# Performance work log

Measured on AMD Instinct MI355X. Metric: run time of the kernel, lower is better.

Reference implementation:

```python
import jax, jax.numpy as jnp
import numpy as np

B, S, D, H, FF = 4, 1024, 1024, 16, 4096
DH = D // H
EPS = 1e-5


def setup_inputs() -> dict:
    key = jax.random.key(0)
    ks = jax.random.split(key, 24)
    w = lambda i, shp: jax.random.normal(ks[i], shp, jnp.float32) * 0.02
    inp = {
        'tgt': jax.random.normal(ks[0], (B, S, D), jnp.float32),
        'memory': jax.random.normal(ks[1], (B, S, D), jnp.float32),
        'mask': jax.random.randint(ks[2], (B, S, S), 0, 2, jnp.int32),
        # self-attention projections (stored [in,out]; torch Linear weight transposed)
        'sa_wq': w(3, (D, D)), 'sa_bq': jnp.zeros((D,), jnp.float32),
        'sa_wk': w(4, (D, D)), 'sa_bk': jnp.zeros((D,), jnp.float32),
        'sa_wv': w(5, (D, D)), 'sa_bv': jnp.zeros((D,), jnp.float32),
        'sa_wo': w(6, (D, D)), 'sa_bo': jnp.zeros((D,), jnp.float32),
        # cross-attention projections
        'ca_wq': w(7, (D, D)), 'ca_bq': jnp.zeros((D,), jnp.float32),
        'ca_wk': w(8, (D, D)), 'ca_bk': jnp.zeros((D,), jnp.float32),
        'ca_wv': w(9, (D, D)), 'ca_bv': jnp.zeros((D,), jnp.float32),
        'ca_wo': w(10, (D, D)), 'ca_bo': jnp.zeros((D,), jnp.float32),
        # FFN
        'w1': w(11, (D, FF)), 'b1': jnp.zeros((FF,), jnp.float32),
        'w2': w(12, (FF, D)), 'b2': jnp.zeros((D,), jnp.float32),
        # LayerNorms
        'g1': jnp.ones((D,), jnp.float32), 'be1': jnp.zeros((D,), jnp.float32),
        'g2': jnp.ones((D,), jnp.float32), 'be2': jnp.zeros((D,), jnp.float32),
        'g3': jnp.ones((D,), jnp.float32), 'be3': jnp.zeros((D,), jnp.float32),
    }
    return inp


def _layernorm(x, g, b):
    m = jnp.mean(x, axis=-1, keepdims=True)
    v = jnp.mean((x - m) ** 2, axis=-1, keepdims=True)
    return (x - m) * jax.lax.rsqrt(v + EPS) * g + b


def _mha(x, y, mask, wq, bq, wk, bk, wv, bv, wo, bo):
    # chunk(h,-1)+cat(0) head-split == reshape to [B,S,H,DH]
    b_, sq, _ = x.shape
    sk = y.shape[1]
    q = (x @ wq + bq).reshape(b_, sq, H, DH)
    k = (y @ wk + bk).reshape(b_, sk, H, DH)
    v = (y @ wv + bv).reshape(b_, sk, H, DH)
    score = jnp.einsum('bqhd,bkhd->bhqk', q, k) / jnp.float32(np.sqrt(DH))
    score = score + (1.0 - mask[:, None].astype(score.dtype)) * (-1e9)
    attn = jax.nn.softmax(score, axis=-1)
    out = jnp.einsum('bhqk,bkhd->bqhd', attn, v).reshape(b_, sq, D)
    return out @ wo + bo


def reference(tgt, memory, mask,
              sa_wq, sa_bq, sa_wk, sa_bk, sa_wv, sa_bv, sa_wo, sa_bo,
              ca_wq, ca_bq, ca_wk, ca_bk, ca_wv, ca_bv, ca_wo, ca_bo,
              w1, b1, w2, b2, g1, be1, g2, be2, g3, be3):
    t = tgt + _mha(tgt, tgt, mask, sa_wq, sa_bq, sa_wk, sa_bk, sa_wv, sa_bv, sa_wo, sa_bo)
    t = _layernorm(t, g1, be1)
    t = t + _mha(t, memory, mask, ca_wq, ca_bq, ca_wk, ca_bk, ca_wv, ca_bv, ca_wo, ca_bo)
    t = _layernorm(t, g2, be2)
    t = t + (jax.nn.relu(t @ w1 + b1) @ w2 + b2)
    t = _layernorm(t, g3, be3)
    return t
```

## Files before the change

kernel.cpp:

```cpp
#include <hip/hip_runtime.h>
#include <math.h>

typedef float f32x4 __attribute__((ext_vector_type(4)));
typedef unsigned short ushort8 __attribute__((ext_vector_type(8)));
typedef unsigned short ushort4v __attribute__((ext_vector_type(4)));
typedef __bf16 bf16x8 __attribute__((ext_vector_type(8)));
typedef unsigned int u32;

__device__ __forceinline__ unsigned short f2bf(float x) {
  union { float f; unsigned u; } v; v.f = x;
  unsigned r = v.u + 0x7FFFu + ((v.u >> 16) & 1u);
  return (unsigned short)(r >> 16);
}
__device__ __forceinline__ float bf2f(unsigned short u) {
  union { unsigned u; float f; } c; c.u = ((unsigned)u) << 16; return c.f;
}

__device__ __forceinline__ f32x4 mfma16(ushort8 a, ushort8 b, f32x4 c) {
  return __builtin_amdgcn_mfma_f32_16x16x32_bf16(
      __builtin_bit_cast(bf16x8, a), __builtin_bit_cast(bf16x8, b), c, 0, 0, 0);
}

__device__ __forceinline__ void gload16(const void* g, void* l) {
  __builtin_amdgcn_global_load_lds((const __attribute__((address_space(1))) u32*)g,
                                   (__attribute__((address_space(3))) u32*)l, 16, 0, 0);
}

__global__ __launch_bounds__(256) void gemm_bf16_kernel(
    const unsigned short* __restrict__ A, const unsigned short* __restrict__ Bt,
    const float* __restrict__ bias, void* __restrict__ C,
    int M, int N, int K, int flags)
{
  __shared__ __align__(16) char As0[128 * 128];
  __shared__ __align__(16) char Bs0[128 * 128];
  __shared__ __align__(16) char As1[128 * 128];
  __shared__ __align__(16) char Bs1[128 * 128];
  const int bn = blockIdx.x, bm = blockIdx.y;
  const int t = threadIdx.x;
  const int lane = t & 63, w = t >> 6, wm = w >> 1, wn = w & 1;
  const int l4 = lane & 15, lg = lane >> 4;
  const size_t K2 = (size_t)K * 2;

  f32x4 acc[4][4];
#pragma unroll
  for (int i = 0; i < 4; ++i)
#pragma unroll
    for (int j = 0; j < 4; ++j) acc[i][j] = f32x4{0.f, 0.f, 0.f, 0.f};

  const int lr = lane >> 3;
  const int ls = (lane & 7) ^ lr;
  const char* Ag = (const char*)A + (size_t)(bm * 128 + w * 32 + lr) * K2 + ls * 16;
  const char* Bg = (const char*)Bt + (size_t)(bn * 128 + w * 32 + lr) * K2 + ls * 16;
  const int wo = w * 4096;

  auto STAGE = [&](char* Al, char* Bl, int kt) {
    const size_t ko = (size_t)kt * 128;
#pragma unroll
    for (int i = 0; i < 4; ++i) {
      gload16(Ag + i * 8 * K2 + ko, Al + wo + i * 1024);
      gload16(Bg + i * 8 * K2 + ko, Bl + wo + i * 1024);
    }
  };
  auto COMPUTE = [&](const char* As, const char* Bs) {
#pragma unroll
    for (int ks = 0; ks < 2; ++ks) {
      const int kb = ks * 64 + lg * 16;
      ushort8 af[4], bfr[4];
#pragma unroll
      for (int mi = 0; mi < 4; ++mi) {
        int r = wm * 64 + mi * 16 + l4;
        af[mi] = *reinterpret_cast<const ushort8*>(As + r * 128 + (kb ^ ((r & 7) << 4)));
      }
#pragma unroll
      for (int ni = 0; ni < 4; ++ni) {
        int r = wn * 64 + ni * 16 + l4;
        bfr[ni] = *reinterpret_cast<const ushort8*>(Bs + r * 128 + (kb ^ ((r & 7) << 4)));
      }
#pragma unroll
      for (int mi = 0; mi < 4; ++mi)
#pragma unroll
        for (int ni = 0; ni < 4; ++ni)
          acc[mi][ni] = mfma16(af[mi], bfr[ni], acc[mi][ni]);
    }
  };

  const int nkt = K >> 6;
  STAGE(As0, Bs0, 0);
  __syncthreads();
  for (int kt = 0; kt < nkt; kt += 2) {
    STAGE(As1, Bs1, kt + 1);
    COMPUTE(As0, Bs0);
    __syncthreads();
    if (kt + 2 < nkt) STAGE(As0, Bs0, kt + 2);
    COMPUTE(As1, Bs1);
    __syncthreads();
  }

  const int relu = flags & 1, obf = flags & 2;
#pragma unroll
  for (int mi = 0; mi < 4; ++mi)
#pragma unroll
    for (int ni = 0; ni < 4; ++ni) {
      int col = bn * 128 + wn * 64 + ni * 16 + l4;
      float bia = bias[col];
#pragma unroll
      for (int j = 0; j < 4; ++j) {
        int row = bm * 128 + wm * 64 + mi * 16 + lg * 4 + j;
        float vv = acc[mi][ni][j] + bia;
        if (relu) vv = fmaxf(vv, 0.f);
        if (obf) ((unsigned short*)C)[(size_t)row * N + col] = f2bf(vv);
        else     ((float*)C)[(size_t)row * N + col] = vv;
      }
    }
}

constexpr int kS = 1024, kD = 1024, kDH = 64;

__global__ __launch_bounds__(256) void attn_kernel(
    const unsigned short* __restrict__ Qg, const unsigned short* __restrict__ Kg,
    const unsigned short* __restrict__ Vg, int qs, int ks_,
    const unsigned short* __restrict__ mpack, unsigned short* __restrict__ Og)
{
  __shared__ __align__(16) char Ks0[8192];
  __shared__ __align__(16) char Ks1[8192];
  __shared__ __align__(16) char VT0[8192];
  __shared__ __align__(16) char VT1[8192];
  __shared__ __align__(16) char Ps[8192];
  const int qt = blockIdx.x, h = blockIdx.y, b = blockIdx.z;
  const int t = threadIdx.x, lane = t & 63, w = t >> 6;
  const int l4 = lane & 15, lg = lane >> 4;
  const int lr = lane >> 3, sg = (lane & 7) ^ lr;

  ushort8 q0, q1;
  {
    const unsigned short* src = Qg + (size_t)(b * kS + qt * 64 + w * 16 + l4) * qs + h * kDH;
    q0 = *reinterpret_cast<const ushort8*>(src + lg * 8);
    q1 = *reinterpret_cast<const ushort8*>(src + 32 + lg * 8);
  }
  const unsigned short* mtb = mpack + (size_t)(b * 16 + qt) * 4096 + t;

  auto stageK = [&](char* Kl, int kt) {
    const char* base = (const char*)(Kg + (size_t)(b * kS + kt * 64) * ks_ + h * kDH) + sg * 16;
    gload16(base + (size_t)(w * 16 + lr) * (ks_ * 2), Kl + w * 2048);
    gload16(base + (size_t)(w * 16 + 8 + lr) * (ks_ * 2), Kl + w * 2048 + 1024);
  };

  float m_r[4], l_p[4];
  f32x4 o[4];
#pragma unroll
  for (int j = 0; j < 4; ++j) { m_r[j] = -1e30f; l_p[j] = 0.f; }
#pragma unroll
  for (int di = 0; di < 4; ++di) o[di] = f32x4{0.f, 0.f, 0.f, 0.f};

  ushort8 vA0, vA1, vB0, vB1;
  unsigned short mA, mB;
  stageK(Ks0, 0);
  {
    const unsigned short* vsrc = Vg + (size_t)(b * kS + (t >> 2)) * ks_ + h * kDH + (t & 3) * 16;
    vA0 = *reinterpret_cast<const ushort8*>(vsrc);
    vA1 = *reinterpret_cast<const ushort8*>(vsrc + 8);
    mA = mtb[0];
  }

#define ATTN_TILE(KC, VC, KN, VC0, VC1, VN0, VN1, MCUR, MNXT, KTV)                       \
  {                                                                                      \
    asm volatile("s_waitcnt vmcnt(0)" ::: "memory");                                     \
    {       \
      int key2 = (t >> 2) * 2, c0 = (t & 3) * 16;                                        \
      _Pragma("unroll")                                                                  \
      for (int i = 0; i < 8; ++i) {                                                      \
        int dh = c0 + i;                                                                 \
        *(unsigned short*)(VC + dh * 128 +                                               \
            (key2 ^ ((dh & 7) << 4) ^ ((dh >> 4) << 5))) = VC0[i];                       \
      }                                                                                  \
      _Pragma("unroll")                                                                  \
      for (int i = 0; i < 8; ++i) {                                                      \
        int dh = c0 + 8 + i;                                                             \
        *(unsigned short*)(VC + dh * 128 +                                               \
            (key2 ^ ((dh & 7) << 4) ^ ((dh >> 4) << 5))) = VC1[i];                       \
      }                                                                                  \
    }                                                                                    \
    asm volatile("s_waitcnt lgkmcnt(0)" ::: "memory");                                   \
    __builtin_amdgcn_s_barrier();                                                        \
    __builtin_amdgcn_sched_barrier(0);                                                   \
    if ((KTV) + 1 < 16) {                  \
      stageK(KN, (KTV) + 1);                                                             \
      const unsigned short* vsrc = Vg +                                                  \
          (size_t)(b * kS + ((KTV) + 1) * 64 + (t >> 2)) * ks_ + h * kDH + (t & 3) * 16; \
      VN0 = *reinterpret_cast<const ushort8*>(vsrc);                                     \
      VN1 = *reinterpret_cast<const ushort8*>(vsrc + 8);                                 \
      MNXT = mtb[((KTV) + 1) * 256];                                                     \
    }                                                                                    \
    f32x4 sc[4];                                                                         \
    _Pragma("unroll")                                                                    \
    for (int ni = 0; ni < 4; ++ni) sc[ni] = f32x4{0.f, 0.f, 0.f, 0.f};                   \
    __builtin_amdgcn_s_setprio(1);                                                       \
    _Pragma("unroll")                                                                    \
    for (int ks = 0; ks < 2; ++ks) {                                                     \
      const int kb = ks * 64 + lg * 16;                                                  \
      ushort8 a = ks ? q1 : q0;                                                          \
      _Pragma("unroll")                                                                  \
      for (int ni = 0; ni < 4; ++ni) {                                                   \
        int kr = ni * 16 + l4;                                                           \
        ushort8 bb = *(const ushort8*)(KC + kr * 128 + (kb ^ ((kr & 7) << 4)));          \
        sc[ni] = mfma16(a, bb, sc[ni]);                                                  \
      }                                                                                  \
    }                                                                                    \
    __builtin_amdgcn_s_setprio(0);                                                       \
    const unsigned mbits_ = (unsigned)(MCUR);                                            \
    float tmax[4];                                                                       \
    _Pragma("unroll")                                                                    \
    for (int j = 0; j < 4; ++j) {                                                        \
      _Pragma("unroll")                                                                  \
      for (int ni = 0; ni < 4; ++ni)                                                     \
        if (!((mbits_ >> (ni * 4 + j)) & 1u)) sc[ni][j] = -1e9f;                         \
      tmax[j] = fmaxf(fmaxf(sc[0][j], sc[1][j]), fmaxf(sc[2][j], sc[3][j]));             \
    }                                                                                    \
    bool need = (tmax[0] > m_r[0] + 8.f) || (tmax[1] > m_r[1] + 8.f) ||                  \
                (tmax[2] > m_r[2] + 8.f) || (tmax[3] > m_r[3] + 8.f);                    \
    if (__any(need)) {                 \
      _Pragma("unroll")                                                                  \
      for (int j = 0; j < 4; ++j) {                                                      \
        tmax[j] = fmaxf(tmax[j], __shfl_xor(tmax[j], 1, 64));                            \
        tmax[j] = fmaxf(tmax[j], __shfl_xor(tmax[j], 2, 64));                            \
        tmax[j] = fmaxf(tmax[j], __shfl_xor(tmax[j], 4, 64));                            \
        tmax[j] = fmaxf(tmax[j], __shfl_xor(tmax[j], 8, 64));                            \
        float mn = fmaxf(m_r[j], tmax[j]);                                               \
        float al = exp2f(m_r[j] - mn);                                                   \
        m_r[j] = mn; l_p[j] *= al;                                                       \
        o[0][j] *= al; o[1][j] *= al; o[2][j] *= al; o[3][j] *= al;                      \
      }                                                                                  \
    }                                                                                    \
    _Pragma("unroll")                                                                    \
    for (int ni = 0; ni < 4; ++ni)                                                       \
      _Pragma("unroll")                                                                  \
      for (int j = 0; j < 4; ++j) {                                                      \
        float p = exp2f(sc[ni][j] - m_r[j]);                                             \
        sc[ni][j] = p;                                                                   \
        l_p[j] += p;                                                                     \
      }                                                                                  \
    {                               \
      char* Pw = Ps + w * 2048;                                                          \
      _Pragma("unroll")                                                                  \
      for (int ni = 0; ni < 4; ++ni)                                                     \
        _Pragma("unroll")                                                                \
        for (int j = 0; j < 4; ++j) {                                                    \
          int row = lg * 4 + j, col = ni * 16 + l4;                                      \
          *(unsigned short*)(Pw + row * 128 +                                            \
              ((col * 2) ^ ((row & 7) << 4) ^ ((row & 8) << 2))) =                       \
              __builtin_bit_cast(unsigned short, (__bf16)sc[ni][j]);                     \
        }                                                                                \
    }                                                                                    \
    asm volatile("s_waitcnt lgkmcnt(0)" ::: "memory");                                   \
    __builtin_amdgcn_sched_barrier(0);                                                   \
    __builtin_amdgcn_s_setprio(1);                                                       \
    {                      \
      const char* Pw = Ps + w * 2048;                                                    \
      _Pragma("unroll")                                                                  \
      for (int ks = 0; ks < 2; ++ks) {                                                   \
        const int kb = ks * 64 + lg * 16;                                                \
        ushort8 pa = *(const ushort8*)(Pw + l4 * 128 +                                   \
            (kb ^ ((l4 & 7) << 4) ^ ((l4 & 8) << 2)));                                   \
        _Pragma("unroll")                                                                \
        for (int di = 0; di < 4; ++di) {                                                 \
          int vr2 = di * 16 + l4;                                                        \
          ushort8 vb = *(const ushort8*)(VC + vr2 * 128 +                                \
              (kb ^ ((vr2 & 7) << 4) ^ ((vr2 >> 4) << 5)));                              \
          o[di] = mfma16(pa, vb, o[di]);                                                 \
        }                                                                                \
      }                                                                                  \
    }                                                                                    \
    __builtin_amdgcn_s_setprio(0);                                                       \
  }

  for (int kt = 0; kt < 16; kt += 2) {
    ATTN_TILE(Ks0, VT0, Ks1, vA0, vA1, vB0, vB1, mA, mB, kt);
    ATTN_TILE(Ks1, VT1, Ks0, vB0, vB1, vA0, vA1, mB, mA, kt + 1);
  }
#undef ATTN_TILE

  float rinv[4];
#pragma unroll
  for (int j = 0; j < 4; ++j) {
    float s = l_p[j];
    s += __shfl_xor(s, 1, 64);
    s += __shfl_xor(s, 2, 64);
    s += __shfl_xor(s, 4, 64);
    s += __shfl_xor(s, 8, 64);
    rinv[j] = 1.0f / s;
  }
#pragma unroll
  for (int di = 0; di < 4; ++di) {
    int col = h * kDH + di * 16 + l4;
#pragma unroll
    for (int j = 0; j < 4; ++j) {
      int qrow = qt * 64 + w * 16 + lg * 4 + j;
      Og[(size_t)(b * kS + qrow) * kD + col] =
          __builtin_bit_cast(unsigned short, (__bf16)(o[di][j] * rinv[j]));
    }
  }
}

__global__ __launch_bounds__(256) void addln_kernel(
    const float* __restrict__ x, const unsigned short* __restrict__ y,
    const float* __restrict__ g, const float* __restrict__ be,
    float* __restrict__ out, unsigned short* __restrict__ ob)
{
  const int row = blockIdx.x, t = threadIdx.x;
  const size_t base = (size_t)row * 1024 + t * 4;
  float4 xv = *reinterpret_cast<const float4*>(x + base);
  ushort4v yv = *reinterpret_cast<const ushort4v*>(y + base);
  float v0 = xv.x + bf2f(yv[0]), v1 = xv.y + bf2f(yv[1]);
  float v2 = xv.z + bf2f(yv[2]), v3 = xv.w + bf2f(yv[3]);
  float s1 = v0 + v1 + v2 + v3;
  float s2 = v0 * v0 + v1 * v1 + v2 * v2 + v3 * v3;
#pragma unroll
  for (int off = 1; off < 64; off <<= 1) {
    s1 += __shfl_xor(s1, off, 64);
    s2 += __shfl_xor(s2, off, 64);
  }
  __shared__ float r1[4], r2[4];
  const int w = t >> 6, lane = t & 63;
  if (lane == 0) { r1[w] = s1; r2[w] = s2; }
  __syncthreads();
  s1 = r1[0] + r1[1] + r1[2] + r1[3];
  s2 = r2[0] + r2[1] + r2[2] + r2[3];
  const float mean = s1 * (1.0f / 1024.0f);
  const float var = s2 * (1.0f / 1024.0f) - mean * mean;
  const float rs = rsqrtf(var + 1e-5f);
  float4 gv = *reinterpret_cast<const float4*>(g + t * 4);
  float4 bv = *reinterpret_cast<const float4*>(be + t * 4);
  float4 ov;
  ov.x = (v0 - mean) * rs * gv.x + bv.x;
  ov.y = (v1 - mean) * rs * gv.y + bv.y;
  ov.z = (v2 - mean) * rs * gv.z + bv.z;
  ov.w = (v3 - mean) * rs * gv.w + bv.w;
  *reinterpret_cast<float4*>(out + base) = ov;
  if (ob) {
    ushort4v bo;
    bo[0] = f2bf(ov.x); bo[1] = f2bf(ov.y); bo[2] = f2bf(ov.z); bo[3] = f2bf(ov.w);
    *reinterpret_cast<ushort4v*>(ob + base) = bo;
  }
}

__global__ __launch_bounds__(256) void cvt2_bf16_kernel(
    const float* __restrict__ a, const float* __restrict__ b,
    unsigned short* __restrict__ da, unsigned short* __restrict__ db, int n8each)
{
  int i = blockIdx.x * 256 + threadIdx.x;
  const float* s = a; unsigned short* d = da;
  if (i >= n8each) { s = b; d = db; i -= n8each; }
  if (i >= n8each) return;
  float4 f0 = reinterpret_cast<const float4*>(s)[i * 2];
  float4 f1 = reinterpret_cast<const float4*>(s)[i * 2 + 1];
  ushort8 v;
  v[0] = f2bf(f0.x); v[1] = f2bf(f0.y); v[2] = f2bf(f0.z); v[3] = f2bf(f0.w);
  v[4] = f2bf(f1.x); v[5] = f2bf(f1.y); v[6] = f2bf(f1.z); v[7] = f2bf(f1.w);
  reinterpret_cast<ushort8*>(d)[i] = v;
}

__global__ __launch_bounds__(256) void transpose_cvt_kernel(
    const float* __restrict__ src, unsigned short* __restrict__ dst, int K, int N)
{
  __shared__ float tile[32][33];
  const int bx = blockIdx.x, by = blockIdx.y;
  const int tx = threadIdx.x & 31, ty = threadIdx.x >> 5;
#pragma unroll
  for (int i = 0; i < 4; ++i)
    tile[ty + i * 8][tx] = src[(size_t)(by * 32 + ty + i * 8) * N + bx * 32 + tx];
  __syncthreads();
#pragma unroll
  for (int i = 0; i < 4; ++i)
    dst[(size_t)(bx * 32 + ty + i * 8) * K + by * 32 + tx] = f2bf(tile[tx][ty + i * 8]);
}

struct TPtrs { const float* s[8]; unsigned short* d[8]; float scale[8]; };
__global__ __launch_bounds__(256) void tcvt_batch_kernel(TPtrs p)
{
  __shared__ float tile[32][33];
  const float* __restrict__ src = p.s[blockIdx.z];
  unsigned short* __restrict__ dst = p.d[blockIdx.z];
  const float sc = p.scale[blockIdx.z];
  const int bx = blockIdx.x, by = blockIdx.y;
  const int tx = threadIdx.x & 31, ty = threadIdx.x >> 5;
#pragma unroll
  for (int i = 0; i < 4; ++i)
    tile[ty + i * 8][tx] = src[(size_t)(by * 32 + ty + i * 8) * 1024 + bx * 32 + tx];
  __syncthreads();
#pragma unroll
  for (int i = 0; i < 4; ++i)
    dst[(size_t)(bx * 32 + ty + i * 8) * 1024 + by * 32 + tx] = f2bf(tile[tx][ty + i * 8] * sc);
}

__global__ void biasprep_kernel(const float* sq, const float* sk, const float* sv,
                                const float* cq, const float* ck, const float* cv,
                                float* bsa, float* bca, float* bcq, float s)
{
  int i = blockIdx.x * 256 + threadIdx.x;
  if (i < 1024) { bsa[i] = sq[i] * s; bcq[i] = cq[i] * s; bca[i] = ck[i]; bca[i + 1024] = cv[i]; }
  else if (i < 2048) bsa[i] = sk[i - 1024];
  else if (i < 3072) bsa[i] = sv[i - 2048];
}

__global__ __launch_bounds__(256) void maskprep_kernel(
    const int* __restrict__ mask, unsigned short* __restrict__ mpack)
{
  int idx = blockIdx.x * 256 + threadIdx.x;
  int t = idx & 255;
  int kt = (idx >> 8) & 15;
  int qt = (idx >> 12) & 15;
  int b = idx >> 16;
  int qb = qt * 64 + ((t >> 6) & 3) * 16 + ((t >> 4) & 3) * 4;
  int kb = kt * 64 + (t & 15);
  unsigned m = 0;
#pragma unroll
  for (int ni = 0; ni < 4; ++ni)
#pragma unroll
    for (int j = 0; j < 4; ++j)
      if (mask[(size_t)(b * 1024 + qb + j) * 1024 + kb + ni * 16]) m |= 1u << (ni * 4 + j);
  mpack[idx] = (unsigned short)m;
}

extern "C" void kernel_launch(void* const* d_in, const int* in_sizes, int n_in,
                              void* d_out, int out_size, void* d_ws, size_t ws_size,
                              hipStream_t stream)
{
  const float* tgt  = (const float*)d_in[0];
  const float* memi = (const float*)d_in[1];
  const int*   mask = (const int*)d_in[2];
  const float* sa_wq = (const float*)d_in[3];  const float* sa_bq = (const float*)d_in[4];
  const float* sa_wk = (const float*)d_in[5];  const float* sa_bk = (const float*)d_in[6];
  const float* sa_wv = (const float*)d_in[7];  const float* sa_bv = (const float*)d_in[8];
  const float* sa_wo = (const float*)d_in[9];  const float* sa_bo = (const float*)d_in[10];
  const float* ca_wq = (const float*)d_in[11]; const float* ca_bq = (const float*)d_in[12];
  const float* ca_wk = (const float*)d_in[13]; const float* ca_bk = (const float*)d_in[14];
  const float* ca_wv = (const float*)d_in[15]; const float* ca_bv = (const float*)d_in[16];
  const float* ca_wo = (const float*)d_in[17]; const float* ca_bo = (const float*)d_in[18];
  const float* w1 = (const float*)d_in[19]; const float* b1 = (const float*)d_in[20];
  const float* w2 = (const float*)d_in[21]; const float* b2 = (const float*)d_in[22];
  const float* g1 = (const float*)d_in[23]; const float* be1 = (const float*)d_in[24];
  const float* g2 = (const float*)d_in[25]; const float* be2 = (const float*)d_in[26];
  const float* g3 = (const float*)d_in[27]; const float* be3 = (const float*)d_in[28];
  float* out = (float*)d_out;
  char* W = (char*)d_ws;
  const size_t MB = 1 << 20;
  typedef unsigned short us;
  const float QSCALE = 0.18033688011112042f;

  us* Wsaqkv = (us*)(W + 0);
  us* Wsao   = (us*)(W + 6 * MB);
  us* Wcaq   = (us*)(W + 8 * MB);
  us* Wcakv  = (us*)(W + 10 * MB);
  us* Wcao   = (us*)(W + 14 * MB);
  us* W1t    = (us*)(W + 16 * MB);
  us* W2t    = (us*)(W + 24 * MB);
  float* b_saqkv = (float*)(W + 32 * MB);
  float* b_cakv  = (float*)(W + 32 * MB + 16384);
  float* b_caq   = (float*)(W + 32 * MB + 32768);
  us* tgt_bf = (us*)(W + 33 * MB);
  us* T2b    = tgt_bf;
  us* mem_bf = (us*)(W + 41 * MB);
  us* QKV    = (us*)(W + 49 * MB);
  us* Qca    = (us*)(W + 49 * MB);
  us* KVca   = (us*)(W + 57 * MB);
  us* T1b    = (us*)(W + 65 * MB);
  us* AO     = (us*)(W + 73 * MB);
  us* Hb     = (us*)(W + 49 * MB);
  us* Opb    = (us*)(W + 81 * MB);
  us* mpack  = (us*)(W + 89 * MB);
  float* T1f = (float*)(W + 98 * MB);
  float* T2f = T1f;

  const int M = 4096;
  dim3 blk(256);
  auto gemm = [&](const us* Aa, const us* Bta, const float* bias, void* Cc,
                  int Nn, int Kk, int flags) {
    gemm_bf16_kernel<<<dim3(Nn / 128, M / 128), blk, 0, stream>>>(Aa, Bta, bias, Cc, M, Nn, Kk, flags);
  };

  TPtrs tp;
  tp.s[0] = sa_wq; tp.d[0] = Wsaqkv;              tp.scale[0] = QSCALE;
  tp.s[1] = sa_wk; tp.d[1] = Wsaqkv + 1024 * 1024; tp.scale[1] = 1.f;
  tp.s[2] = sa_wv; tp.d[2] = Wsaqkv + 2048 * 1024; tp.scale[2] = 1.f;
  tp.s[3] = sa_wo; tp.d[3] = Wsao;                 tp.scale[3] = 1.f;
  tp.s[4] = ca_wq; tp.d[4] = Wcaq;                 tp.scale[4] = QSCALE;
  tp.s[5] = ca_wk; tp.d[5] = Wcakv;                tp.scale[5] = 1.f;
  tp.s[6] = ca_wv; tp.d[6] = Wcakv + 1024 * 1024;  tp.scale[6] = 1.f;
  tp.s[7] = ca_wo; tp.d[7] = Wcao;                 tp.scale[7] = 1.f;
  tcvt_batch_kernel<<<dim3(32, 32, 8), blk, 0, stream>>>(tp);
  transpose_cvt_kernel<<<dim3(128, 32), blk, 0, stream>>>(w1, W1t, 1024, 4096);
  transpose_cvt_kernel<<<dim3(32, 128), blk, 0, stream>>>(w2, W2t, 4096, 1024);
  cvt2_bf16_kernel<<<dim3(4096), blk, 0, stream>>>(tgt, memi, tgt_bf, mem_bf, M * 1024 / 8);
  biasprep_kernel<<<dim3(12), blk, 0, stream>>>(sa_bq, sa_bk, sa_bv, ca_bq, ca_bk, ca_bv,
                                                b_saqkv, b_cakv, b_caq, QSCALE);
  maskprep_kernel<<<dim3(1024), blk, 0, stream>>>(mask, mpack);

  gemm(tgt_bf, Wsaqkv, b_saqkv, QKV, 3072, 1024, 2);
  attn_kernel<<<dim3(16, 16, 4), blk, 0, stream>>>(QKV, QKV + 1024, QKV + 2048, 3072, 3072, mpack, AO);
  gemm(AO, Wsao, sa_bo, Opb, 1024, 1024, 2);
  addln_kernel<<<dim3(M), blk, 0, stream>>>(tgt, Opb, g1, be1, T1f, T1b);

  gemm(T1b, Wcaq, b_caq, Qca, 1024, 1024, 2);
  gemm(mem_bf, Wcakv, b_cakv, KVca, 2048, 1024, 2);
  attn_kernel<<<dim3(16, 16, 4), blk, 0, stream>>>(Qca, KVca, KVca + 1024, 1024, 2048, mpack, AO);
  gemm(AO, Wcao, ca_bo, Opb, 1024, 1024, 2);
  addln_kernel<<<dim3(M), blk, 0, stream>>>(T1f, Opb, g2, be2, T2f, T2b);

  gemm(T2b, W1t, b1, Hb, 4096, 1024, 3);
  gemm(Hb, W2t, b2, Opb, 1024, 4096, 2);
  addln_kernel<<<dim3(M), blk, 0, stream>>>(T2f, Opb, g3, be3, out, nullptr);

  (void)in_sizes; (void)n_in; (void)out_size; (void)ws_size;
}
```

Baseline: 411.6 us.

## Remap workgroups per XCD and deepen GEMM load pipeline with explicit vmcnt waits

Adds an XCD-aware block index remapping to both the GEMM and attention kernels, so consecutive tiles that share operands land on the same XCD and reuse its L2. The GEMM main loop now issues two stages of global-to-LDS loads ahead and waits with partial s_waitcnt vmcnt instead of full __syncthreads, keeping one tile of loads in flight during compute. This relies on the vmcnt count of 8 matching the number of loads per stage, and the hand-placed barriers carry a risk of LDS races if that assumption does not hold.

```diff
diff --git a/kernel.cpp b/kernel.cpp
--- a/kernel.cpp
+++ b/kernel.cpp
@@ -26,6 +26,12 @@
                                    (__attribute__((address_space(3))) u32*)l, 16, 0, 0);
 }
 
+__device__ __forceinline__ int xcd_swz(int orig, int nwg) {
+  int q = nwg >> 3, r = nwg & 7;
+  int xcd = orig & 7, lid = orig >> 3;
+  return (xcd < r ? xcd * (q + 1) : r * (q + 1) + (xcd - r) * q) + lid;
+}
+
 __global__ __launch_bounds__(256) void gemm_bf16_kernel(
     const unsigned short* __restrict__ A, const unsigned short* __restrict__ Bt,
     const float* __restrict__ bias, void* __restrict__ C,
@@ -35,7 +41,9 @@
   __shared__ __align__(16) char Bs0[128 * 128];
   __shared__ __align__(16) char As1[128 * 128];
   __shared__ __align__(16) char Bs1[128 * 128];
-  const int bn = blockIdx.x, bm = blockIdx.y;
+  const int gx = gridDim.x;
+  const int wg = xcd_swz(blockIdx.x + gx * blockIdx.y, gx * gridDim.y);
+  const int bn = wg % gx, bm = wg / gx;
   const int t = threadIdx.x;
   const int lane = t & 63, w = t >> 6, wm = w >> 1, wn = w & 1;
   const int l4 = lane & 15, lg = lane >> 4;
@@ -84,17 +92,29 @@
     }
   };
 
+#define GWAIT(more) do { if (more) asm volatile("s_waitcnt vmcnt(8)" ::: "memory"); \
+                         else      asm volatile("s_waitcnt vmcnt(0)" ::: "memory"); } while (0)
+
   const int nkt = K >> 6;
   STAGE(As0, Bs0, 0);
-  __syncthreads();
+  STAGE(As1, Bs1, 1);
   for (int kt = 0; kt < nkt; kt += 2) {
-    STAGE(As1, Bs1, kt + 1);
+    GWAIT(kt + 1 < nkt);
+    __builtin_amdgcn_s_barrier();
+    __builtin_amdgcn_sched_barrier(0);
     COMPUTE(As0, Bs0);
-    __syncthreads();
+    __builtin_amdgcn_s_barrier();
+    __builtin_amdgcn_sched_barrier(0);
     if (kt + 2 < nkt) STAGE(As0, Bs0, kt + 2);
+    GWAIT(kt + 2 < nkt);
+    __builtin_amdgcn_s_barrier();
+    __builtin_amdgcn_sched_barrier(0);
     COMPUTE(As1, Bs1);
-    __syncthreads();
-  }
+    __builtin_amdgcn_s_barrier();
+    __builtin_amdgcn_sched_barrier(0);
+    if (kt + 3 < nkt) STAGE(As1, Bs1, kt + 3);
+  }
+#undef GWAIT
 
   const int relu = flags & 1, obf = flags & 2;
 #pragma unroll
@@ -126,7 +146,8 @@
   __shared__ __align__(16) char VT0[8192];
   __shared__ __align__(16) char VT1[8192];
   __shared__ __align__(16) char Ps[8192];
-  const int qt = blockIdx.x, h = blockIdx.y, b = blockIdx.z;
+  const int wg = xcd_swz(blockIdx.x + 16 * (blockIdx.y + 16 * blockIdx.z), 1024);
+  const int qt = wg & 15, h = (wg >> 4) & 15, b = wg >> 8;
   const int t = threadIdx.x, lane = t & 63, w = t >> 6;
   const int l4 = lane & 15, lg = lane >> 4;
   const int lr = lane >> 3, sg = (lane & 7) ^ lr;
```

After: 399.4 us. 1.03x faster.
